# Kernel optimization log

Hardware: AMD Instinct MI355X
Metric: run time of the kernel (lower is better)

Reference implementation:

```python
import jax, jax.numpy as jnp
import numpy as np

N_NODES = 100000


def gcn_conv(x, W, b, row, col, ew, n):
    # PyG GCNConv: out = D^{-1/2} (A + I) D^{-1/2} (x @ W) + b
    xw = x @ W  # [N, out_dim]
    # add self-loops with weight 1
    loops = jnp.arange(n, dtype=row.dtype)
    row2 = jnp.concatenate([row, loops])
    col2 = jnp.concatenate([col, loops])
    ew2 = jnp.concatenate([ew, jnp.ones((n,), dtype=ew.dtype)])
    # degree at target (col) index, symmetric norm
    deg = jax.ops.segment_sum(ew2, col2, num_segments=n)
    dinv = jnp.where(deg > 0, jax.lax.rsqrt(deg), 0.0)
    norm = dinv[row2] * ew2 * dinv[col2]  # [E+N]
    msg = xw[row2] * norm[:, None]        # gather + scale: [E+N, out_dim]
    out = jax.ops.segment_sum(msg, col2, num_segments=n)  # scatter-add at targets
    return out + b


def setup_inputs() -> dict:
    key = jax.random.key(0)
    ks = jax.random.split(key, 10)
    nf, hc1, hc2, nc = 128, 64, 32, 16
    n, e = N_NODES, 1600000
    x = jax.random.normal(ks[0], (n, nf), dtype=jnp.float32)
    edge_index = jax.random.randint(ks[1], (2, e), 0, n, dtype=jnp.int64)
    edge_weight = jax.random.uniform(ks[2], (e,), dtype=jnp.float32)
    def glorot(k, fi, fo):
        s = jnp.sqrt(6.0 / (fi + fo)).astype(jnp.float32)
        return jax.random.uniform(k, (fi, fo), jnp.float32, -s, s)
    return {
        "x": x,
        "edge_index": edge_index,
        "edge_weight": edge_weight,
        "W1": glorot(ks[3], nf, hc1), "b1": jnp.zeros((hc1,), jnp.float32),
        "W2": glorot(ks[4], hc1, hc2), "b2": jnp.zeros((hc2,), jnp.float32),
        "W3": glorot(ks[5], hc2, nc), "b3": jnp.zeros((nc,), jnp.float32),
    }


def reference(x, edge_index, edge_weight, W1, b1, W2, b2, W3, b3):
    n = x.shape[0]
    row, col = edge_index[0], edge_index[1]
    # eval mode: dropout is identity
    h = jnp.tanh(gcn_conv(x, W1, b1, row, col, edge_weight, n))
    emb = gcn_conv(h, W2, b2, row, col, edge_weight, n)
    h_act = jnp.tanh(emb)
    logits = gcn_conv(h_act, W3, b3, row, col, edge_weight, n)
    return (logits, emb)
```

## Files before the change

### kernel.cpp

```cpp
#include <hip/hip_runtime.h>
#include <cstdint>


#define BNODES 512
#define CAPB   8704
#define L1CHUNK 2048

typedef unsigned long long u64;
typedef unsigned int u32;

static __device__ __forceinline__ unsigned short f2bf(float f) {
    u32 u = __float_as_uint(f);
    u += 0x7fffu + ((u >> 16) & 1u);
    return (unsigned short)(u >> 16);
}
static __device__ __forceinline__ float bflo(u32 q) { return __uint_as_float(q << 16); }
static __device__ __forceinline__ float bfhi(u32 q) { return __uint_as_float(q & 0xffff0000u); }

__global__ __launch_bounds__(256)
void k_lvl1(const int* __restrict__ rowi, const int* __restrict__ coli,
            const float* __restrict__ ew, int* __restrict__ gcursor,
            u64* __restrict__ gbucket, int E, int B) {
    __shared__ u64 lbuf[L1CHUNK];
    __shared__ unsigned short bbuf[L1CHUNK];
    __shared__ int hist[256], excl[256], cursor[256], gbase[256];

    const int t = threadIdx.x;
    const int base = blockIdx.x * L1CHUNK;
    const int nval = min(L1CHUNK, E - base);

    hist[t] = 0;
    __syncthreads();

    u64 pk[8]; int bk[8];
    #pragma unroll
    for (int k = 0; k < 8; k++) {
        int i = k * 256 + t;
        int e = base + i;
        bk[k] = -1;
        if (i < nval) {
            int r = rowi[e], c = coli[e];
            float w = ew[e];
            int b = c >> 9;
            bk[k] = b;
            pk[k] = ((u64)r << 41) | ((u64)(c & 511) << 32) | (u64)__float_as_uint(w);
            atomicAdd(&hist[b], 1);
        }
    }
    __syncthreads();

    int s = hist[t];
    int x = s;
    __shared__ int scanb[256];
    scanb[t] = x;
    __syncthreads();
    for (int off = 1; off < 256; off <<= 1) {
        int y = (t >= off) ? scanb[t - off] : 0;
        __syncthreads();
        x += y;
        scanb[t] = x;
        __syncthreads();
    }
    excl[t] = x - s;
    cursor[t] = x - s;
    if (t < B && s > 0) gbase[t] = atomicAdd(&gcursor[t], s);
    __syncthreads();

    #pragma unroll
    for (int k = 0; k < 8; k++) {
        if (bk[k] >= 0) {
            int pos = atomicAdd(&cursor[bk[k]], 1);
            lbuf[pos] = pk[k];
            bbuf[pos] = (unsigned short)bk[k];
        }
    }
    __syncthreads();

    for (int p = t; p < nval; p += 256) {
        int b = bbuf[p];
        int dst = gbase[b] + (p - excl[b]);
        if (dst < CAPB)
            gbucket[(size_t)b * CAPB + dst] = lbuf[p];
    }
}

__global__ __launch_bounds__(512)
void k_lvl2(const int* __restrict__ gcursor, u64* __restrict__ gbucket,
            float* __restrict__ dinv, u32* __restrict__ rowinfo, int n) {
    __shared__ u64 ebuf[CAPB];
    __shared__ int hist[512];
    __shared__ float degw[512];
    __shared__ int scanv[512];
    __shared__ int excl[512], cur[512];

    const int t = threadIdx.x;
    const int b = blockIdx.x;
    const int cnt = min(gcursor[b], CAPB);
    u64* bucket = gbucket + (size_t)b * CAPB;

    hist[t] = 0;
    degw[t] = 0.f;
    __syncthreads();

    for (int i = t; i < cnt; i += 512) {
        u64 p = bucket[i];
        ebuf[i] = p;
        int cl = (int)((p >> 32) & 511);
        float w = __uint_as_float((u32)p);
        atomicAdd(&hist[cl], 1);
        atomicAdd(&degw[cl], w);
    }
    __syncthreads();

    int s = hist[t];
    int x = s;
    scanv[t] = x;
    __syncthreads();
    for (int off = 1; off < 512; off <<= 1) {
        int y = (t >= off) ? scanv[t - off] : 0;
        __syncthreads();
        x += y;
        scanv[t] = x;
        __syncthreads();
    }
    excl[t] = x - s;
    cur[t] = x - s;

    int j = b * BNODES + t;
    if (j < n) {
        dinv[j] = rsqrtf(degw[t] + 1.0f);
        u32 start = (u32)(b * CAPB + (x - s));
        rowinfo[j] = (start << 8) | (u32)min(s, 255);
    }
    __syncthreads();

    int2* out = (int2*)bucket;
    for (int i = t; i < cnt; i += 512) {
        u64 p = ebuf[i];
        int cl = (int)((p >> 32) & 511);
        int pos = atomicAdd(&cur[cl], 1);
        out[pos] = make_int2((int)(p >> 41), (int)(u32)p);
    }
}

template<int IN, int OUT, int RPT, bool TANH_IN>
__global__ __launch_bounds__(256)
void k_gemm(const float* __restrict__ X, const float* __restrict__ W,
            const float* __restrict__ dinv, unsigned short* __restrict__ Y, int n) {
    constexpr int CG = OUT / 4;
    constexpr int RSLOTS = 256 / CG;
    constexpr int TILE = RSLOTS * RPT;
    constexpr int XPITCH = IN + 4;

    __shared__ float Wl[IN * OUT];
    __shared__ float Xl[TILE][XPITCH];

    for (int j = threadIdx.x; j < IN * OUT / 4; j += 256)
        reinterpret_cast<float4*>(Wl)[j] = reinterpret_cast<const float4*>(W)[j];

    const int cg = threadIdx.x % CG;
    const int rs = threadIdx.x / CG;
    const int ntiles = (n + TILE - 1) / TILE;

    for (int tile = blockIdx.x; tile < ntiles; tile += gridDim.x) {
        const int row0 = tile * TILE;
        __syncthreads();
        for (int j = threadIdx.x; j < TILE * IN / 4; j += 256) {
            int fl = j * 4;
            int r = fl / IN, k = fl % IN;
            int gr = row0 + r;
            float4 v = make_float4(0.f, 0.f, 0.f, 0.f);
            if (gr < n) v = reinterpret_cast<const float4*>(X)[(gr * IN + k) >> 2];
            if (TANH_IN) { v.x = tanhf(v.x); v.y = tanhf(v.y); v.z = tanhf(v.z); v.w = tanhf(v.w); }
            *reinterpret_cast<float4*>(&Xl[r][k]) = v;
        }
        __syncthreads();

        float4 acc[RPT];
        #pragma unroll
        for (int r = 0; r < RPT; r++) acc[r] = make_float4(0.f, 0.f, 0.f, 0.f);

        #pragma unroll 4
        for (int k = 0; k < IN; k++) {
            float4 w4 = *reinterpret_cast<const float4*>(&Wl[k * OUT + cg * 4]);
            #pragma unroll
            for (int r = 0; r < RPT; r++) {
                float xv = Xl[rs * RPT + r][k];
                acc[r].x += xv * w4.x;
                acc[r].y += xv * w4.y;
                acc[r].z += xv * w4.z;
                acc[r].w += xv * w4.w;
            }
        }

        #pragma unroll
        for (int r = 0; r < RPT; r++) {
            int gr = row0 + rs * RPT + r;
            if (gr < n) {
                float di = dinv[gr];
                ushort4 o;
                o.x = f2bf(di * acc[r].x);
                o.y = f2bf(di * acc[r].y);
                o.z = f2bf(di * acc[r].z);
                o.w = f2bf(di * acc[r].w);
                reinterpret_cast<ushort4*>(Y)[(gr * OUT + cg * 4) >> 2] = o;
            }
        }
    }
}

template<int OUT, bool TANH>
__global__ __launch_bounds__(256)
void k_gather(const unsigned short* __restrict__ Y, const u32* __restrict__ rowinfo,
              const int2* __restrict__ epack,
              const float* __restrict__ dinv, const float* __restrict__ b,
              float* __restrict__ out, int n) {
    constexpr int TPE = OUT / 8;
    constexpr int EPW = 64 / TPE;
    const int wid  = threadIdx.x >> 6;
    const int lane = threadIdx.x & 63;
    const int g = lane / TPE;
    const int t = lane % TPE;
    const int c = blockIdx.x * 4 + wid;
    if (c >= n) return;

    const uint4* Y4 = reinterpret_cast<const uint4*>(Y);
    const u32 ri = rowinfo[c];
    const int base = (int)(ri >> 8);
    const int end  = base + (int)(ri & 255);

    float acc[8];
    #pragma unroll
    for (int k = 0; k < 8; k++) acc[k] = 0.f;

    for (int p0 = base; p0 < end; p0 += EPW) {
        int p = p0 + g;
        if (p < end) {
            int2 rw = epack[p];
            float w = __int_as_float(rw.y);
            uint4 q = Y4[(size_t)rw.x * TPE + t];
            acc[0] += w * bflo(q.x); acc[1] += w * bfhi(q.x);
            acc[2] += w * bflo(q.y); acc[3] += w * bfhi(q.y);
            acc[4] += w * bflo(q.z); acc[5] += w * bfhi(q.z);
            acc[6] += w * bflo(q.w); acc[7] += w * bfhi(q.w);
        }
    }
    #pragma unroll
    for (int off = TPE; off < 64; off <<= 1) {
        #pragma unroll
        for (int k = 0; k < 8; k++) acc[k] += __shfl_xor(acc[k], off, 64);
    }
    if (g == 0) {
        uint4 q = Y4[(size_t)c * TPE + t];
        float self[8] = { bflo(q.x), bfhi(q.x), bflo(q.y), bfhi(q.y),
                          bflo(q.z), bfhi(q.z), bflo(q.w), bfhi(q.w) };
        float4 b0 = reinterpret_cast<const float4*>(b)[2 * t];
        float4 b1 = reinterpret_cast<const float4*>(b)[2 * t + 1];
        float bb[8] = { b0.x, b0.y, b0.z, b0.w, b1.x, b1.y, b1.z, b1.w };
        float di = dinv[c];
        float o[8];
        #pragma unroll
        for (int k = 0; k < 8; k++) {
            o[k] = di * (acc[k] + self[k]) + bb[k];
            if (TANH) o[k] = tanhf(o[k]);
        }
        float4* dst = reinterpret_cast<float4*>(out + (size_t)c * OUT + t * 8);
        dst[0] = make_float4(o[0], o[1], o[2], o[3]);
        dst[1] = make_float4(o[4], o[5], o[6], o[7]);
    }
}

extern "C" void kernel_launch(void* const* d_in, const int* in_sizes, int n_in,
                              void* d_out, int out_size, void* d_ws, size_t ws_size,
                              hipStream_t stream) {
    const float* x  = (const float*)d_in[0];
    const int*   ei = (const int*)d_in[1];
    const float* ew = (const float*)d_in[2];
    const float* W1 = (const float*)d_in[3];
    const float* b1 = (const float*)d_in[4];
    const float* W2 = (const float*)d_in[5];
    const float* b2 = (const float*)d_in[6];
    const float* W3 = (const float*)d_in[7];
    const float* b3 = (const float*)d_in[8];

    const int E = in_sizes[2];
    const int n = in_sizes[0] / 128;

    const int* rowi = ei;
    const int* coli = ei + E;

    const int B = (n + BNODES - 1) / BNODES;

    float* wsf     = (float*)d_ws;
    float* dinv    = wsf;
    unsigned short* yb = (unsigned short*)(wsf + (size_t)n);
    float* h       = wsf + (size_t)33 * n;
    u32*   rowinfo = (u32*)(wsf + (size_t)97 * n);
    u64*   gbucket = (u64*)(wsf + (size_t)98 * n);
    int*   gcursor = (int*)(wsf + (size_t)98 * n + (size_t)2 * B * CAPB);

    float* logits = (float*)d_out;
    float* emb    = (float*)d_out + (size_t)16 * n;

    const int TB = 256;
    auto cdiv = [](long long a, long long b) { return (int)((a + b - 1) / b); };

    hipMemsetAsync(gcursor, 0, (size_t)B * 4, stream);
    k_lvl1<<<cdiv(E, L1CHUNK), TB, 0, stream>>>(rowi, coli, ew, gcursor, gbucket, E, B);
    k_lvl2<<<B, 512, 0, stream>>>(gcursor, gbucket, dinv, rowinfo, n);
    const int2* epack = (const int2*)gbucket;

    k_gemm<128, 64, 2, false><<<2048, TB, 0, stream>>>(x, W1, dinv, yb, n);
    k_gather<64, true><<<cdiv(n, 4), TB, 0, stream>>>(yb, rowinfo, epack, dinv, b1, h, n);

    k_gemm<64, 32, 2, false><<<2048, TB, 0, stream>>>(h, W2, dinv, yb, n);
    k_gather<32, false><<<cdiv(n, 4), TB, 0, stream>>>(yb, rowinfo, epack, dinv, b2, emb, n);

    k_gemm<32, 16, 2, true><<<2048, TB, 0, stream>>>(emb, W3, dinv, yb, n);
    k_gather<16, false><<<cdiv(n, 4), TB, 0, stream>>>(yb, rowinfo, epack, dinv, b3, logits, n);
}
```

Before: 344.6 us.

## Assign one node per thread group in gather instead of one per wavefront

The gather kernel now maps each group of TPE lanes to its own destination node, so a wavefront handles several nodes at once instead of splitting one node's edges across groups and reducing with shuffles. This drops the cross-lane shuffle reduction and the idle lanes that appear when a node has fewer edges than groups, and the grid shrinks to match. The edge loop is unrolled by two so two gathers are in flight. The cost is load imbalance inside a wavefront, since nodes with different degrees now run in lockstep, and edge-list reads are no longer coalesced across groups.

New measurement: 297.2 us. 13.8% less time.

```diff
diff --git a/kernel.cpp b/kernel.cpp
--- a/kernel.cpp
+++ b/kernel.cpp
@@ -216,58 +216,64 @@
               const float* __restrict__ dinv, const float* __restrict__ b,
               float* __restrict__ out, int n) {
     constexpr int TPE = OUT / 8;
-    constexpr int EPW = 64 / TPE;
+    constexpr int NPW = 64 / TPE;
     const int wid  = threadIdx.x >> 6;
     const int lane = threadIdx.x & 63;
     const int g = lane / TPE;
     const int t = lane % TPE;
-    const int c = blockIdx.x * 4 + wid;
+    const int c = (blockIdx.x * 4 + wid) * NPW + g;
     if (c >= n) return;
 
     const uint4* Y4 = reinterpret_cast<const uint4*>(Y);
     const u32 ri = rowinfo[c];
-    const int base = (int)(ri >> 8);
-    const int end  = base + (int)(ri & 255);
-
-    float acc[8];
+    const int2* ep = epack + (ri >> 8);
+    const int cnt = (int)(ri & 255);
+
+    float acc[8] = {0.f, 0.f, 0.f, 0.f, 0.f, 0.f, 0.f, 0.f};
+
+    int i = 0;
+    for (; i + 2 <= cnt; i += 2) {
+        int2 rw0 = ep[i];
+        int2 rw1 = ep[i + 1];
+        float w0 = __int_as_float(rw0.y);
+        float w1 = __int_as_float(rw1.y);
+        uint4 q0 = Y4[(size_t)rw0.x * TPE + t];
+        uint4 q1 = Y4[(size_t)rw1.x * TPE + t];
+        acc[0] += w0 * bflo(q0.x); acc[1] += w0 * bfhi(q0.x);
+        acc[2] += w0 * bflo(q0.y); acc[3] += w0 * bfhi(q0.y);
+        acc[4] += w0 * bflo(q0.z); acc[5] += w0 * bfhi(q0.z);
+        acc[6] += w0 * bflo(q0.w); acc[7] += w0 * bfhi(q0.w);
+        acc[0] += w1 * bflo(q1.x); acc[1] += w1 * bfhi(q1.x);
+        acc[2] += w1 * bflo(q1.y); acc[3] += w1 * bfhi(q1.y);
+        acc[4] += w1 * bflo(q1.z); acc[5] += w1 * bfhi(q1.z);
+        acc[6] += w1 * bflo(q1.w); acc[7] += w1 * bfhi(q1.w);
+    }
+    if (i < cnt) {
+        int2 rw = ep[i];
+        float w = __int_as_float(rw.y);
+        uint4 q = Y4[(size_t)rw.x * TPE + t];
+        acc[0] += w * bflo(q.x); acc[1] += w * bfhi(q.x);
+        acc[2] += w * bflo(q.y); acc[3] += w * bfhi(q.y);
+        acc[4] += w * bflo(q.z); acc[5] += w * bfhi(q.z);
+        acc[6] += w * bflo(q.w); acc[7] += w * bfhi(q.w);
+    }
+
+    uint4 q = Y4[(size_t)c * TPE + t];
+    float self[8] = { bflo(q.x), bfhi(q.x), bflo(q.y), bfhi(q.y),
+                      bflo(q.z), bfhi(q.z), bflo(q.w), bfhi(q.w) };
+    float4 b0 = reinterpret_cast<const float4*>(b)[2 * t];
+    float4 b1 = reinterpret_cast<const float4*>(b)[2 * t + 1];
+    float bb[8] = { b0.x, b0.y, b0.z, b0.w, b1.x, b1.y, b1.z, b1.w };
+    float di = dinv[c];
+    float o[8];
     #pragma unroll
-    for (int k = 0; k < 8; k++) acc[k] = 0.f;
-
-    for (int p0 = base; p0 < end; p0 += EPW) {
-        int p = p0 + g;
-        if (p < end) {
-            int2 rw = epack[p];
-            float w = __int_as_float(rw.y);
-            uint4 q = Y4[(size_t)rw.x * TPE + t];
-            acc[0] += w * bflo(q.x); acc[1] += w * bfhi(q.x);
-            acc[2] += w * bflo(q.y); acc[3] += w * bfhi(q.y);
-            acc[4] += w * bflo(q.z); acc[5] += w * bfhi(q.z);
-            acc[6] += w * bflo(q.w); acc[7] += w * bfhi(q.w);
-        }
-    }
-    #pragma unroll
-    for (int off = TPE; off < 64; off <<= 1) {
-        #pragma unroll
-        for (int k = 0; k < 8; k++) acc[k] += __shfl_xor(acc[k], off, 64);
-    }
-    if (g == 0) {
-        uint4 q = Y4[(size_t)c * TPE + t];
-        float self[8] = { bflo(q.x), bfhi(q.x), bflo(q.y), bfhi(q.y),
-                          bflo(q.z), bfhi(q.z), bflo(q.w), bfhi(q.w) };
-        float4 b0 = reinterpret_cast<const float4*>(b)[2 * t];
-        float4 b1 = reinterpret_cast<const float4*>(b)[2 * t + 1];
-        float bb[8] = { b0.x, b0.y, b0.z, b0.w, b1.x, b1.y, b1.z, b1.w };
-        float di = dinv[c];
-        float o[8];
-        #pragma unroll
-        for (int k = 0; k < 8; k++) {
-            o[k] = di * (acc[k] + self[k]) + bb[k];
-            if (TANH) o[k] = tanhf(o[k]);
-        }
-        float4* dst = reinterpret_cast<float4*>(out + (size_t)c * OUT + t * 8);
-        dst[0] = make_float4(o[0], o[1], o[2], o[3]);
-        dst[1] = make_float4(o[4], o[5], o[6], o[7]);
-    }
+    for (int k = 0; k < 8; k++) {
+        o[k] = di * (acc[k] + self[k]) + bb[k];
+        if (TANH) o[k] = tanhf(o[k]);
+    }
+    float4* dst = reinterpret_cast<float4*>(out + (size_t)c * OUT + t * 8);
+    dst[0] = make_float4(o[0], o[1], o[2], o[3]);
+    dst[1] = make_float4(o[4], o[5], o[6], o[7]);
 }
 
 extern "C" void kernel_launch(void* const* d_in, const int* in_sizes, int n_in,
@@ -311,11 +317,11 @@
     const int2* epack = (const int2*)gbucket;
 
     k_gemm<128, 64, 2, false><<<2048, TB, 0, stream>>>(x, W1, dinv, yb, n);
-    k_gather<64, true><<<cdiv(n, 4), TB, 0, stream>>>(yb, rowinfo, epack, dinv, b1, h, n);
+    k_gather<64, true><<<cdiv(n, 32), TB, 0, stream>>>(yb, rowinfo, epack, dinv, b1, h, n);
 
     k_gemm<64, 32, 2, false><<<2048, TB, 0, stream>>>(h, W2, dinv, yb, n);
-    k_gather<32, false><<<cdiv(n, 4), TB, 0, stream>>>(yb, rowinfo, epack, dinv, b2, emb, n);
+    k_gather<32, false><<<cdiv(n, 64), TB, 0, stream>>>(yb, rowinfo, epack, dinv, b2, emb, n);
 
     k_gemm<32, 16, 2, true><<<2048, TB, 0, stream>>>(emb, W3, dinv, yb, n);
-    k_gather<16, false><<<cdiv(n, 4), TB, 0, stream>>>(yb, rowinfo, epack, dinv, b3, logits, n);
-}
+    k_gather<16, false><<<cdiv(n, 128), TB, 0, stream>>>(yb, rowinfo, epack, dinv, b3, logits, n);
+}
```
